# Optimization experiments

Measured on AMD Instinct MI355X. Metric: run time of the kernel, lower is better.

Reference implementation:

```python
import jax, jax.numpy as jnp
import numpy as np

N_NODES = 50000
N_EDGES = 800000
N_GRAPHS = 64
IN_DIM, HID1, HID2, N_CLASSES = 128, 256, 128, 10


def setup_inputs() -> dict:
    key = jax.random.key(0)
    ks = jax.random.split(key, 12)
    x = jax.random.normal(ks[0], (N_NODES, IN_DIM), dtype=jnp.float32)
    src = jax.random.randint(ks[1], (N_EDGES,), 0, N_NODES, dtype=jnp.int32)
    dst = jax.random.randint(ks[2], (N_EDGES,), 0, N_NODES, dtype=jnp.int32)
    graph_id = jnp.sort(jax.random.randint(ks[3], (N_NODES,), 0, N_GRAPHS, dtype=jnp.int32))
    s1 = 1.0 / np.sqrt(IN_DIM)
    s2 = 1.0 / np.sqrt(HID1)
    s3 = 1.0 / np.sqrt(HID2)
    s4 = 1.0 / np.sqrt(12)
    return {
        'x': x, 'src': src, 'dst': dst, 'graph_id': graph_id,
        'W1': jax.random.normal(ks[4], (IN_DIM, HID1), dtype=jnp.float32) * s1,
        'b1': jnp.zeros((HID1,), dtype=jnp.float32),
        'W2': jax.random.normal(ks[5], (HID1, HID2), dtype=jnp.float32) * s2,
        'b2': jnp.zeros((HID2,), dtype=jnp.float32),
        'Wc1': jax.random.normal(ks[6], (HID2, 12), dtype=jnp.float32) * s3,
        'bc1': jnp.zeros((12,), dtype=jnp.float32),
        'Wc2': jax.random.normal(ks[7], (12, 12), dtype=jnp.float32) * s4,
        'bc2': jnp.zeros((12,), dtype=jnp.float32),
        'Wc3': jax.random.normal(ks[8], (12, N_CLASSES), dtype=jnp.float32) * s4,
        'bc3': jnp.zeros((N_CLASSES,), dtype=jnp.float32),
    }


def _graph_conv(x, W, b, src, dst, inv_sqrt_out, inv_sqrt_in, n_nodes):
    # DGL GraphConv, norm='both': D_out^{-1/2} applied to source feats,
    # sum-aggregate over edges, then D_in^{-1/2} on destination, then +bias.
    # Weight applied first (equivalent by linearity; reduces gather traffic
    # when out_dim < in_dim, and is exactly what DGL does in that case).
    xw = (x * inv_sqrt_out[:, None]) @ W                      # [N, out]
    agg = jax.ops.segment_sum(xw[src], dst, num_segments=n_nodes)  # SpMM
    return agg * inv_sqrt_in[:, None] + b


def reference(x, src, dst, graph_id, W1, b1, W2, b2, Wc1, bc1, Wc2, bc2, Wc3, bc3):
    n = x.shape[0]
    ones_e = jnp.ones(src.shape, dtype=x.dtype)
    deg_out = jnp.maximum(jax.ops.segment_sum(ones_e, src, num_segments=n), 1.0)
    deg_in = jnp.maximum(jax.ops.segment_sum(ones_e, dst, num_segments=n), 1.0)
    inv_o = jax.lax.rsqrt(deg_out)
    inv_i = jax.lax.rsqrt(deg_in)

    h = jax.nn.relu(_graph_conv(x, W1, b1, src, dst, inv_o, inv_i, n))
    h = jax.nn.relu(_graph_conv(h, W2, b2, src, dst, inv_o, inv_i, n))

    # dgl.mean_nodes: per-graph mean over nodes of the batched graph
    gsum = jax.ops.segment_sum(h, graph_id, num_segments=N_GRAPHS)   # [G, HID2]
    cnt = jnp.maximum(jax.ops.segment_sum(jnp.ones((n,), dtype=h.dtype), graph_id, num_segments=N_GRAPHS), 1.0)
    hg = gsum / cnt[:, None]

    # tiny 3-layer MLP (no activations in between, as in the source)
    out = hg @ Wc1 + bc1
    out = out @ Wc2 + bc2
    out = out @ Wc3 + bc3
    return out
```

## Files before the change

kernel.cpp:

```cpp
#include <hip/hip_runtime.h>
#include <hip/hip_bf16.h>

#define IN_DIM 128
#define HID1 256
#define HID2 128

#define HB_BINS 25000
#define HB_WORDS 12500
#define HB_CHUNKS 64
__global__ __launch_bounds__(256) void hist_count(const int* __restrict__ src,
                                                  const int* __restrict__ dst,
                                                  int E, int chunk_size,
                                                  int* __restrict__ part_in,
                                                  int* __restrict__ part_out, int N) {
    __shared__ int sm[HB_WORDS];
    const int* idx = (blockIdx.z == 0) ? dst : src;
    int* part = (blockIdx.z == 0) ? part_in : part_out;
    const int base = blockIdx.y * HB_BINS;
    const int ebeg = blockIdx.x * chunk_size;
    const int eend = min(ebeg + chunk_size, E);
    for (int w = threadIdx.x; w < HB_WORDS; w += 256) sm[w] = 0;
    __syncthreads();
    for (int e = ebeg + threadIdx.x; e < eend; e += 256) {
        int v = idx[e] - base;
        if ((unsigned)v < (unsigned)HB_BINS)
            atomicAdd(&sm[v >> 1], 1 << ((v & 1) * 16));
    }
    __syncthreads();
    const int nb = min(HB_BINS, N - base);
    int* dp = part + (size_t)blockIdx.x * N + base;
    for (int w = threadIdx.x; 2 * w < nb; w += 256) {
        int packed = sm[w];
        int b = 2 * w;
        dp[b] = packed & 0xffff;
        if (b + 1 < nb) dp[b + 1] = (packed >> 16) & 0xffff;
    }
}

__global__ __launch_bounds__(256) void hist_reduce(const int* __restrict__ part_in,
                                                   const int* __restrict__ part_out,
                                                   int N, int* __restrict__ deg_in,
                                                   float* __restrict__ inv_i,
                                                   float* __restrict__ inv_o) {
    int b = blockIdx.x * blockDim.x + threadIdx.x;
    if (b >= N) return;
    int di = 0, dox = 0;
#pragma unroll 4
    for (int k = 0; k < HB_CHUNKS; ++k) {
        di += part_in[(size_t)k * N + b];
        dox += part_out[(size_t)k * N + b];
    }
    deg_in[b] = di;
    inv_i[b] = rsqrtf((float)max(di, 1));
    inv_o[b] = rsqrtf((float)max(dox, 1));
}

#define SCAN_B 256
__global__ __launch_bounds__(SCAN_B) void scan_partial(const int* __restrict__ deg,
                                                       int* __restrict__ blockSums, int n) {
    __shared__ int sm[SCAN_B];
    int i = blockIdx.x * SCAN_B + threadIdx.x;
    int v = (i < n) ? deg[i] : 0;
    sm[threadIdx.x] = v;
    __syncthreads();
#pragma unroll
    for (int off = SCAN_B / 2; off > 0; off >>= 1) {
        if (threadIdx.x < off) sm[threadIdx.x] += sm[threadIdx.x + off];
        __syncthreads();
    }
    if (threadIdx.x == 0) blockSums[blockIdx.x] = sm[0];
}

__global__ __launch_bounds__(SCAN_B) void scan_blocksums(int* __restrict__ blockSums, int nb) {
    __shared__ int sm[SCAN_B];
    int t = threadIdx.x;
    int v = (t < nb) ? blockSums[t] : 0;
    sm[t] = v;
    __syncthreads();
#pragma unroll
    for (int off = 1; off < SCAN_B; off <<= 1) {
        int u = (t >= off) ? sm[t - off] : 0;
        __syncthreads();
        sm[t] += u;
        __syncthreads();
    }
    if (t < nb) blockSums[t] = sm[t] - v;
}

__global__ __launch_bounds__(SCAN_B) void scan_final(const int* __restrict__ deg,
                                                     const int* __restrict__ blockSums,
                                                     int* __restrict__ row, int n) {
    __shared__ int sm[SCAN_B];
    int i = blockIdx.x * SCAN_B + threadIdx.x;
    int v = (i < n) ? deg[i] : 0;
    sm[threadIdx.x] = v;
    __syncthreads();
#pragma unroll
    for (int off = 1; off < SCAN_B; off <<= 1) {
        int u = (threadIdx.x >= off) ? sm[threadIdx.x - off] : 0;
        __syncthreads();
        sm[threadIdx.x] += u;
        __syncthreads();
    }
    int excl = sm[threadIdx.x] - v + blockSums[blockIdx.x];
    if (i < n) {
        row[i] = excl;
        if (i == n - 1) row[n] = excl + v;
    }
}

#define BK_SHIFT 8
#define NBUCK 196
#define NCHUNK 256
__global__ __launch_bounds__(256) void coarse_hist(const int* __restrict__ dst, int E,
                                                   int chunk_size, int* __restrict__ ccnt) {
    __shared__ int cnt[NBUCK];
    for (int i = threadIdx.x; i < NBUCK; i += 256) cnt[i] = 0;
    __syncthreads();
    int ebeg = blockIdx.x * chunk_size, eend = min(ebeg + chunk_size, E);
    for (int e = ebeg + threadIdx.x; e < eend; e += 256)
        atomicAdd(&cnt[dst[e] >> BK_SHIFT], 1);
    __syncthreads();
    for (int i = threadIdx.x; i < NBUCK; i += 256) ccnt[blockIdx.x * NBUCK + i] = cnt[i];
}

__global__ __launch_bounds__(NCHUNK) void coarse_off(const int* __restrict__ ccnt,
                                                     const int* __restrict__ row, int N,
                                                     int* __restrict__ coff) {
    __shared__ int sm[NCHUNK];
    int b = blockIdx.x, t = threadIdx.x;
    int v = ccnt[t * NBUCK + b];
    sm[t] = v;
    __syncthreads();
#pragma unroll
    for (int off = 1; off < NCHUNK; off <<= 1) {
        int u = (t >= off) ? sm[t - off] : 0;
        __syncthreads();
        sm[t] += u;
        __syncthreads();
    }
    int base = row[min(b << BK_SHIFT, N)];
    coff[t * NBUCK + b] = base + sm[t] - v;
}

__global__ __launch_bounds__(256) void scat_a(const int* __restrict__ src,
                                              const int* __restrict__ dst, int E,
                                              int chunk_size, const int* __restrict__ coff,
                                              int2* __restrict__ pairs) {
    __shared__ int lcur[NBUCK];
    for (int i = threadIdx.x; i < NBUCK; i += 256) lcur[i] = coff[blockIdx.x * NBUCK + i];
    __syncthreads();
    int ebeg = blockIdx.x * chunk_size, eend = min(ebeg + chunk_size, E);
    for (int e = ebeg + threadIdx.x; e < eend; e += 256) {
        int d = dst[e];
        int p = atomicAdd(&lcur[d >> BK_SHIFT], 1);
        pairs[p] = make_int2(src[e], d);
    }
}

__global__ __launch_bounds__(256) void scat_b(const int2* __restrict__ pairs,
                                              const int* __restrict__ row, int N,
                                              int* __restrict__ csr_src) {
    __shared__ int cur[1 << BK_SHIFT];
    const int nb0 = blockIdx.x << BK_SHIFT;
    const int nb1 = min(nb0 + (1 << BK_SHIFT), N);
    if (nb0 >= N) return;
    for (int i = threadIdx.x; i < nb1 - nb0; i += 256) cur[i] = row[nb0 + i];
    __syncthreads();
    const int beg = row[nb0], end = row[nb1];
    for (int j = beg + threadIdx.x; j < end; j += 256) {
        int2 pr = pairs[j];
        int p = atomicAdd(&cur[pr.y - nb0], 1);
        csr_src[p] = pr.x;
    }
}

__global__ void cvt_kernel(const float* __restrict__ in, __hip_bfloat16* __restrict__ out, int n4) {
    int i = blockIdx.x * blockDim.x + threadIdx.x;
    if (i < n4) {
        float4 v = reinterpret_cast<const float4*>(in)[i];
        __hip_bfloat16 b0 = __float2bfloat16(v.x);
        __hip_bfloat16 b1 = __float2bfloat16(v.y);
        __hip_bfloat16 b2 = __float2bfloat16(v.z);
        __hip_bfloat16 b3 = __float2bfloat16(v.w);
        ushort4 o = make_ushort4(*(unsigned short*)&b0, *(unsigned short*)&b1,
                                 *(unsigned short*)&b2, *(unsigned short*)&b3);
        reinterpret_cast<ushort4*>(out)[i] = o;
    }
}

__global__ void cvt_transpose_kernel(const float* __restrict__ W, __hip_bfloat16* __restrict__ Wt,
                                     int K, int N) {
    int idx = blockIdx.x * blockDim.x + threadIdx.x;
    if (idx < K * N) {
        int k = idx / N;
        int n = idx - k * N;
        Wt[n * K + k] = __float2bfloat16(W[idx]);
    }
}

__device__ __forceinline__ void bf2_unpack(unsigned int p, float& lo, float& hi) {
    lo = __uint_as_float(p << 16);
    hi = __uint_as_float(p & 0xffff0000u);
}

__global__ __launch_bounds__(256) void spmm_kernel(const __hip_bfloat16* __restrict__ feat,
                                                   const float* __restrict__ scale,
                                                   const int* __restrict__ row,
                                                   const int* __restrict__ csr_src,
                                                   __hip_bfloat16* __restrict__ out_bf,
                                                   float* __restrict__ out_f32, int N) {
    const int node = blockIdx.x * 4 + (threadIdx.x >> 6);
    if (node >= N) return;
    const int lane = threadIdx.x & 63;
    const unsigned int* fp = (const unsigned int*)feat;
    const int beg = row[node];
    const int end = row[node + 1];
    float a0 = 0.f, a1 = 0.f;
    int j = beg;
    if (scale) {
        for (; j + 4 <= end; j += 4) {
            int s0 = csr_src[j], s1 = csr_src[j + 1], s2 = csr_src[j + 2], s3 = csr_src[j + 3];
            unsigned int p0 = fp[(size_t)s0 * 64 + lane];
            unsigned int p1 = fp[(size_t)s1 * 64 + lane];
            unsigned int p2 = fp[(size_t)s2 * 64 + lane];
            unsigned int p3 = fp[(size_t)s3 * 64 + lane];
            float c0 = scale[s0], c1 = scale[s1], c2 = scale[s2], c3 = scale[s3];
            float lo, hi;
            bf2_unpack(p0, lo, hi); a0 += lo * c0; a1 += hi * c0;
            bf2_unpack(p1, lo, hi); a0 += lo * c1; a1 += hi * c1;
            bf2_unpack(p2, lo, hi); a0 += lo * c2; a1 += hi * c2;
            bf2_unpack(p3, lo, hi); a0 += lo * c3; a1 += hi * c3;
        }
        for (; j < end; ++j) {
            int s0 = csr_src[j];
            unsigned int p0 = fp[(size_t)s0 * 64 + lane];
            float c0 = scale[s0], lo, hi;
            bf2_unpack(p0, lo, hi); a0 += lo * c0; a1 += hi * c0;
        }
    } else {
        for (; j + 4 <= end; j += 4) {
            int s0 = csr_src[j], s1 = csr_src[j + 1], s2 = csr_src[j + 2], s3 = csr_src[j + 3];
            unsigned int p0 = fp[(size_t)s0 * 64 + lane];
            unsigned int p1 = fp[(size_t)s1 * 64 + lane];
            unsigned int p2 = fp[(size_t)s2 * 64 + lane];
            unsigned int p3 = fp[(size_t)s3 * 64 + lane];
            float lo, hi;
            bf2_unpack(p0, lo, hi); a0 += lo; a1 += hi;
            bf2_unpack(p1, lo, hi); a0 += lo; a1 += hi;
            bf2_unpack(p2, lo, hi); a0 += lo; a1 += hi;
            bf2_unpack(p3, lo, hi); a0 += lo; a1 += hi;
        }
        for (; j < end; ++j) {
            unsigned int p0 = fp[(size_t)csr_src[j] * 64 + lane];
            float lo, hi;
            bf2_unpack(p0, lo, hi); a0 += lo; a1 += hi;
        }
    }
    if (out_bf) {
        __hip_bfloat16 b0 = __float2bfloat16(a0);
        __hip_bfloat16 b1 = __float2bfloat16(a1);
        unsigned int packed = (unsigned int)(*(unsigned short*)&b0) |
                              ((unsigned int)(*(unsigned short*)&b1) << 16);
        ((unsigned int*)out_bf)[(size_t)node * 64 + lane] = packed;
    } else {
        float2 o = make_float2(a0, a1);
        ((float2*)out_f32)[(size_t)node * 64 + lane] = o;
    }
}

#define GBM 128
#define GBN 128
#define GBK 32
#define LPAD 40
typedef __attribute__((ext_vector_type(4))) float floatx4;
typedef __attribute__((ext_vector_type(8))) short shortx8;

__global__ __launch_bounds__(256) void mfma_gemm_kernel(const __hip_bfloat16* __restrict__ A,
                                                        const __hip_bfloat16* __restrict__ Bt,
                                                        __hip_bfloat16* __restrict__ C,
                                                        const float* __restrict__ scaleR,
                                                        const float* __restrict__ bias,
                                                        const float* __restrict__ scaleO,
                                                        int M, int Nn, int K, int doRelu) {
    __shared__ __align__(16) __hip_bfloat16 As[GBM * LPAD];
    __shared__ __align__(16) __hip_bfloat16 Bs[GBN * LPAD];
    const int tid = threadIdx.x;
    const int bm = blockIdx.x * GBM;
    const int bn = blockIdx.y * GBN;
    const int wid = tid >> 6;
    const int lane = tid & 63;
    const int wm = (wid & 1) * 64;
    const int wn = (wid >> 1) * 64;
    const int lrow = lane & 15;
    const int quad = lane >> 4;

    floatx4 acc[4][4] = {};

    for (int k0 = 0; k0 < K; k0 += GBK) {
#pragma unroll
        for (int it = 0; it < 2; ++it) {
            int slot = tid + (it << 8);
            int r = slot >> 2;
            int c = (slot & 3) << 3;
            int gr = bm + r;
            float4 v = make_float4(0.f, 0.f, 0.f, 0.f);
            if (gr < M) v = *reinterpret_cast<const float4*>(A + (size_t)gr * K + k0 + c);
            *reinterpret_cast<float4*>(&As[r * LPAD + c]) = v;
        }
#pragma unroll
        for (int it = 0; it < 2; ++it) {
            int slot = tid + (it << 8);
            int r = slot >> 2;
            int c = (slot & 3) << 3;
            float4 v = *reinterpret_cast<const float4*>(Bt + (size_t)(bn + r) * K + k0 + c);
            *reinterpret_cast<float4*>(&Bs[r * LPAD + c]) = v;
        }
        __syncthreads();

        shortx8 af[4], bf[4];
#pragma unroll
        for (int i = 0; i < 4; ++i)
            af[i] = *reinterpret_cast<const shortx8*>(&As[(wm + i * 16 + lrow) * LPAD + quad * 8]);
#pragma unroll
        for (int i = 0; i < 4; ++i)
            bf[i] = *reinterpret_cast<const shortx8*>(&Bs[(wn + i * 16 + lrow) * LPAD + quad * 8]);
#pragma unroll
        for (int im = 0; im < 4; ++im)
#pragma unroll
            for (int in = 0; in < 4; ++in)
                acc[im][in] = __builtin_amdgcn_mfma_f32_16x16x32_bf16(af[im], bf[in], acc[im][in], 0, 0, 0);
        __syncthreads();
    }

    float bv[4];
#pragma unroll
    for (int in = 0; in < 4; ++in)
        bv[in] = bias ? bias[bn + wn + in * 16 + lrow] : 0.f;

#pragma unroll
    for (int im = 0; im < 4; ++im) {
#pragma unroll
        for (int reg = 0; reg < 4; ++reg) {
            int r = bm + wm + im * 16 + quad * 4 + reg;
            if (r >= M) continue;
            float sR = scaleR ? scaleR[r] : 1.f;
            float sO = scaleO ? scaleO[r] : 1.f;
#pragma unroll
            for (int in = 0; in < 4; ++in) {
                int c = bn + wn + in * 16 + lrow;
                float v = acc[im][in][reg] * sR + bv[in];
                if (doRelu) v = fmaxf(v, 0.f);
                v *= sO;
                C[(size_t)r * Nn + c] = __float2bfloat16(v);
            }
        }
    }
}

#define POOL_CHUNK 64
__global__ __launch_bounds__(128) void pool_kernel(const float* __restrict__ agg2,
                                                   const float* __restrict__ inv_i,
                                                   const float* __restrict__ b2,
                                                   const int* __restrict__ graph_id,
                                                   int n, float* __restrict__ hg_sum) {
    const int f = threadIdx.x;
    const int beg = blockIdx.x * POOL_CHUNK;
    const int end = min(beg + POOL_CHUNK, n);
    if (beg >= n) return;
    const float bias = b2[f];
    int g = graph_id[beg];
    float acc = 0.f;
    for (int i = beg; i < end; ++i) {
        int gi = graph_id[i];
        if (gi != g) {
            atomicAdd(&hg_sum[g * HID2 + f], acc);
            acc = 0.f;
            g = gi;
        }
        float v = agg2[(size_t)i * HID2 + f] * inv_i[i] + bias;
        acc += fmaxf(v, 0.f);
    }
    atomicAdd(&hg_sum[g * HID2 + f], acc);
}

__device__ __forceinline__ int lower_bound_i(const int* a, int n, int key) {
    int lo = 0, hi = n;
    while (lo < hi) {
        int mid = (lo + hi) >> 1;
        if (a[mid] < key) lo = mid + 1; else hi = mid;
    }
    return lo;
}

__global__ __launch_bounds__(64) void mlp_kernel(const float* __restrict__ hg_sum,
                                                 const int* __restrict__ graph_id, int n,
                                                 const float* __restrict__ Wc1, const float* __restrict__ bc1,
                                                 const float* __restrict__ Wc2, const float* __restrict__ bc2,
                                                 const float* __restrict__ Wc3, const float* __restrict__ bc3,
                                                 float* __restrict__ out) {
    const int g = blockIdx.x;
    const int t = threadIdx.x;
    __shared__ float h[HID2];
    __shared__ float t1[12];
    __shared__ float t2[12];
    __shared__ float s_inv_cnt;
    if (t == 0) {
        int beg = lower_bound_i(graph_id, n, g);
        int end = lower_bound_i(graph_id, n, g + 1);
        int c = end - beg;
        s_inv_cnt = 1.0f / (float)max(c, 1);
    }
    __syncthreads();
    const float ic = s_inv_cnt;
    for (int i = t; i < HID2; i += 64) h[i] = hg_sum[g * HID2 + i] * ic;
    __syncthreads();
    if (t < 12) {
        float a = bc1[t];
        for (int k = 0; k < HID2; ++k) a += h[k] * Wc1[k * 12 + t];
        t1[t] = a;
    }
    __syncthreads();
    if (t < 12) {
        float a = bc2[t];
        for (int k = 0; k < 12; ++k) a += t1[k] * Wc2[k * 12 + t];
        t2[t] = a;
    }
    __syncthreads();
    if (t < 10) {
        float a = bc3[t];
        for (int k = 0; k < 12; ++k) a += t2[k] * Wc3[k * 10 + t];
        out[g * 10 + t] = a;
    }
}

extern "C" void kernel_launch(void* const* d_in, const int* in_sizes, int n_in,
                              void* d_out, int out_size, void* d_ws, size_t ws_size,
                              hipStream_t stream) {
    const float* x        = (const float*)d_in[0];
    const int*   src      = (const int*)d_in[1];
    const int*   dst      = (const int*)d_in[2];
    const int*   graph_id = (const int*)d_in[3];
    const float* W1       = (const float*)d_in[4];
    const float* b1       = (const float*)d_in[5];
    const float* W2       = (const float*)d_in[6];
    const float* b2       = (const float*)d_in[7];
    const float* Wc1      = (const float*)d_in[8];
    const float* bc1      = (const float*)d_in[9];
    const float* Wc2      = (const float*)d_in[10];
    const float* bc2      = (const float*)d_in[11];
    const float* Wc3      = (const float*)d_in[12];
    const float* bc3      = (const float*)d_in[13];
    float* out = (float*)d_out;

    const int N = in_sizes[0] / IN_DIM;
    const int E = in_sizes[1];
    const int G = out_size / 10;

    char* ws = (char*)d_ws;
    size_t off = 0;
    auto alloc = [&](size_t bytes) -> char* {
        char* p = ws + off;
        off = (off + bytes + 255) & ~(size_t)255;
        return p;
    };
    const int NB = (N + SCAN_B - 1) / SCAN_B;
    int*   deg_in  = (int*)alloc((size_t)N * 4);
    float* inv_i   = (float*)alloc((size_t)N * 4);
    float* inv_o   = (float*)alloc((size_t)N * 4);
    int*   row     = (int*)alloc((size_t)(N + 1) * 4);
    int*   bsums   = (int*)alloc((size_t)NB * 4);
    int*   ccnt    = (int*)alloc((size_t)NCHUNK * NBUCK * 4);
    int*   coff    = (int*)alloc((size_t)NCHUNK * NBUCK * 4);
    int2*  pairs   = (int2*)alloc((size_t)E * 8);
    int*   csr_src = (int*)alloc((size_t)E * 4);
    float* hg      = (float*)alloc((size_t)G * HID2 * 4);
    __hip_bfloat16* x_bf    = (__hip_bfloat16*)alloc((size_t)N * IN_DIM * 2);
    __hip_bfloat16* W1t     = (__hip_bfloat16*)alloc((size_t)IN_DIM * HID1 * 2);
    __hip_bfloat16* W2t     = (__hip_bfloat16*)alloc((size_t)HID1 * HID2 * 2);
    __hip_bfloat16* agg1_bf = (__hip_bfloat16*)alloc((size_t)N * IN_DIM * 2);
    __hip_bfloat16* h1_bf   = (__hip_bfloat16*)alloc((size_t)N * HID1 * 2);
    __hip_bfloat16* xw2_bf  = (__hip_bfloat16*)alloc((size_t)N * HID2 * 2);
    float* agg2    = (float*)alloc((size_t)N * HID2 * 4);

    int* part_in  = (int*)h1_bf;
    int* part_out = part_in + (size_t)HB_CHUNKS * N;

    hipMemsetAsync(hg, 0, (size_t)G * HID2 * 4, stream);

    const int hchunk = (E + HB_CHUNKS - 1) / HB_CHUNKS;
    const int n_ranges = (N + HB_BINS - 1) / HB_BINS;
    hist_count<<<dim3(HB_CHUNKS, n_ranges, 2), 256, 0, stream>>>(src, dst, E, hchunk,
                                                                 part_in, part_out, N);
    hist_reduce<<<(N + 255) / 256, 256, 0, stream>>>(part_in, part_out, N, deg_in, inv_i, inv_o);
    scan_partial<<<NB, SCAN_B, 0, stream>>>(deg_in, bsums, N);
    scan_blocksums<<<1, SCAN_B, 0, stream>>>(bsums, NB);
    scan_final<<<NB, SCAN_B, 0, stream>>>(deg_in, bsums, row, N);

    const int schunk = (E + NCHUNK - 1) / NCHUNK;
    coarse_hist<<<NCHUNK, 256, 0, stream>>>(dst, E, schunk, ccnt);
    coarse_off<<<NBUCK, NCHUNK, 0, stream>>>(ccnt, row, N, coff);
    scat_a<<<NCHUNK, 256, 0, stream>>>(src, dst, E, schunk, coff, pairs);
    scat_b<<<NBUCK, 256, 0, stream>>>(pairs, row, N, csr_src);

    cvt_kernel<<<(N * IN_DIM / 4 + 255) / 256, 256, 0, stream>>>(x, x_bf, N * IN_DIM / 4);
    cvt_transpose_kernel<<<(IN_DIM * HID1 + 255) / 256, 256, 0, stream>>>(W1, W1t, IN_DIM, HID1);
    cvt_transpose_kernel<<<(HID1 * HID2 + 255) / 256, 256, 0, stream>>>(W2, W2t, HID1, HID2);

    spmm_kernel<<<(N + 3) / 4, 256, 0, stream>>>(x_bf, inv_o, row, csr_src, agg1_bf, nullptr, N);
    mfma_gemm_kernel<<<dim3((N + GBM - 1) / GBM, HID1 / GBN), 256, 0, stream>>>(
        agg1_bf, W1t, h1_bf, inv_i, b1, inv_o, N, HID1, IN_DIM, 1);

    mfma_gemm_kernel<<<dim3((N + GBM - 1) / GBM, HID2 / GBN), 256, 0, stream>>>(
        h1_bf, W2t, xw2_bf, nullptr, nullptr, nullptr, N, HID2, HID1, 0);
    spmm_kernel<<<(N + 3) / 4, 256, 0, stream>>>(xw2_bf, nullptr, row, csr_src, nullptr, agg2, N);

    pool_kernel<<<(N + POOL_CHUNK - 1) / POOL_CHUNK, 128, 0, stream>>>(agg2, inv_i, b2, graph_id, N, hg);
    mlp_kernel<<<G, 64, 0, stream>>>(hg, graph_id, N, Wc1, bc1, Wc2, bc2, Wc3, bc3, out);
}
```

Measured before the change: 305.9 us.

## Fold scale into conversion, fuse scan partial and weight transposes, bf16 agg2

The source-degree scaling moves out of the first SpMM gather and into the x-to-bf16 conversion, so the gather loop no longer loads a per-source scale. The block partial sums of the degree scan are merged into hist_reduce, and the two weight transpose kernels become one launch. The second SpMM now writes bf16 into the reused agg1 buffer instead of a separate fp32 buffer, which halves that write and the pool read. In exchange, agg2 is rounded to bf16 before the final scale, bias and ReLU, which adds a small precision loss.

```diff
diff --git a/kernel.cpp b/kernel.cpp
--- a/kernel.cpp
+++ b/kernel.cpp
@@ -41,36 +41,32 @@
                                                    const int* __restrict__ part_out,
                                                    int N, int* __restrict__ deg_in,
                                                    float* __restrict__ inv_i,
-                                                   float* __restrict__ inv_o) {
-    int b = blockIdx.x * blockDim.x + threadIdx.x;
-    if (b >= N) return;
+                                                   float* __restrict__ inv_o,
+                                                   int* __restrict__ blockSums) {
+    __shared__ int sm[256];
+    int b = blockIdx.x * 256 + threadIdx.x;
     int di = 0, dox = 0;
+    if (b < N) {
 #pragma unroll 4
-    for (int k = 0; k < HB_CHUNKS; ++k) {
-        di += part_in[(size_t)k * N + b];
-        dox += part_out[(size_t)k * N + b];
-    }
-    deg_in[b] = di;
-    inv_i[b] = rsqrtf((float)max(di, 1));
-    inv_o[b] = rsqrtf((float)max(dox, 1));
+        for (int k = 0; k < HB_CHUNKS; ++k) {
+            di += part_in[(size_t)k * N + b];
+            dox += part_out[(size_t)k * N + b];
+        }
+        deg_in[b] = di;
+        inv_i[b] = rsqrtf((float)max(di, 1));
+        inv_o[b] = rsqrtf((float)max(dox, 1));
+    }
+    sm[threadIdx.x] = di;
+    __syncthreads();
+#pragma unroll
+    for (int off = 128; off > 0; off >>= 1) {
+        if (threadIdx.x < off) sm[threadIdx.x] += sm[threadIdx.x + off];
+        __syncthreads();
+    }
+    if (threadIdx.x == 0) blockSums[blockIdx.x] = sm[0];
 }
 
 #define SCAN_B 256
-__global__ __launch_bounds__(SCAN_B) void scan_partial(const int* __restrict__ deg,
-                                                       int* __restrict__ blockSums, int n) {
-    __shared__ int sm[SCAN_B];
-    int i = blockIdx.x * SCAN_B + threadIdx.x;
-    int v = (i < n) ? deg[i] : 0;
-    sm[threadIdx.x] = v;
-    __syncthreads();
-#pragma unroll
-    for (int off = SCAN_B / 2; off > 0; off >>= 1) {
-        if (threadIdx.x < off) sm[threadIdx.x] += sm[threadIdx.x + off];
-        __syncthreads();
-    }
-    if (threadIdx.x == 0) blockSums[blockIdx.x] = sm[0];
-}
-
 __global__ __launch_bounds__(SCAN_B) void scan_blocksums(int* __restrict__ blockSums, int nb) {
     __shared__ int sm[SCAN_B];
     int t = threadIdx.x;
@@ -175,27 +171,34 @@
     }
 }
 
-__global__ void cvt_kernel(const float* __restrict__ in, __hip_bfloat16* __restrict__ out, int n4) {
+__global__ void cvt_scale_kernel(const float* __restrict__ in,
+                                 const float* __restrict__ rowscale,
+                                 __hip_bfloat16* __restrict__ out, int n4) {
     int i = blockIdx.x * blockDim.x + threadIdx.x;
     if (i < n4) {
+        float s = rowscale[i >> 5];
         float4 v = reinterpret_cast<const float4*>(in)[i];
-        __hip_bfloat16 b0 = __float2bfloat16(v.x);
-        __hip_bfloat16 b1 = __float2bfloat16(v.y);
-        __hip_bfloat16 b2 = __float2bfloat16(v.z);
-        __hip_bfloat16 b3 = __float2bfloat16(v.w);
+        __hip_bfloat16 b0 = __float2bfloat16(v.x * s);
+        __hip_bfloat16 b1 = __float2bfloat16(v.y * s);
+        __hip_bfloat16 b2 = __float2bfloat16(v.z * s);
+        __hip_bfloat16 b3 = __float2bfloat16(v.w * s);
         ushort4 o = make_ushort4(*(unsigned short*)&b0, *(unsigned short*)&b1,
                                  *(unsigned short*)&b2, *(unsigned short*)&b3);
         reinterpret_cast<ushort4*>(out)[i] = o;
     }
 }
 
-__global__ void cvt_transpose_kernel(const float* __restrict__ W, __hip_bfloat16* __restrict__ Wt,
-                                     int K, int N) {
+__global__ void cvt_transpose2_kernel(const float* __restrict__ W1, __hip_bfloat16* __restrict__ W1t,
+                                      const float* __restrict__ W2, __hip_bfloat16* __restrict__ W2t) {
     int idx = blockIdx.x * blockDim.x + threadIdx.x;
-    if (idx < K * N) {
-        int k = idx / N;
-        int n = idx - k * N;
-        Wt[n * K + k] = __float2bfloat16(W[idx]);
+    const int S1 = IN_DIM * HID1;
+    if (idx < S1) {
+        int k = idx / HID1, n = idx - k * HID1;
+        W1t[n * IN_DIM + k] = __float2bfloat16(W1[idx]);
+    } else if (idx < S1 + HID1 * HID2) {
+        int j = idx - S1;
+        int k = j / HID2, n = j - k * HID2;
+        W2t[n * HID1 + k] = __float2bfloat16(W2[j]);
     }
 }
 
@@ -205,11 +208,9 @@
 }
 
 __global__ __launch_bounds__(256) void spmm_kernel(const __hip_bfloat16* __restrict__ feat,
-                                                   const float* __restrict__ scale,
                                                    const int* __restrict__ row,
                                                    const int* __restrict__ csr_src,
-                                                   __hip_bfloat16* __restrict__ out_bf,
-                                                   float* __restrict__ out_f32, int N) {
+                                                   __hip_bfloat16* __restrict__ out_bf, int N) {
     const int node = blockIdx.x * 4 + (threadIdx.x >> 6);
     if (node >= N) return;
     const int lane = threadIdx.x & 63;
@@ -218,55 +219,28 @@
     const int end = row[node + 1];
     float a0 = 0.f, a1 = 0.f;
     int j = beg;
-    if (scale) {
-        for (; j + 4 <= end; j += 4) {
-            int s0 = csr_src[j], s1 = csr_src[j + 1], s2 = csr_src[j + 2], s3 = csr_src[j + 3];
-            unsigned int p0 = fp[(size_t)s0 * 64 + lane];
-            unsigned int p1 = fp[(size_t)s1 * 64 + lane];
-            unsigned int p2 = fp[(size_t)s2 * 64 + lane];
-            unsigned int p3 = fp[(size_t)s3 * 64 + lane];
-            float c0 = scale[s0], c1 = scale[s1], c2 = scale[s2], c3 = scale[s3];
-            float lo, hi;
-            bf2_unpack(p0, lo, hi); a0 += lo * c0; a1 += hi * c0;
-            bf2_unpack(p1, lo, hi); a0 += lo * c1; a1 += hi * c1;
-            bf2_unpack(p2, lo, hi); a0 += lo * c2; a1 += hi * c2;
-            bf2_unpack(p3, lo, hi); a0 += lo * c3; a1 += hi * c3;
-        }
-        for (; j < end; ++j) {
-            int s0 = csr_src[j];
-            unsigned int p0 = fp[(size_t)s0 * 64 + lane];
-            float c0 = scale[s0], lo, hi;
-            bf2_unpack(p0, lo, hi); a0 += lo * c0; a1 += hi * c0;
-        }
-    } else {
-        for (; j + 4 <= end; j += 4) {
-            int s0 = csr_src[j], s1 = csr_src[j + 1], s2 = csr_src[j + 2], s3 = csr_src[j + 3];
-            unsigned int p0 = fp[(size_t)s0 * 64 + lane];
-            unsigned int p1 = fp[(size_t)s1 * 64 + lane];
-            unsigned int p2 = fp[(size_t)s2 * 64 + lane];
-            unsigned int p3 = fp[(size_t)s3 * 64 + lane];
-            float lo, hi;
-            bf2_unpack(p0, lo, hi); a0 += lo; a1 += hi;
-            bf2_unpack(p1, lo, hi); a0 += lo; a1 += hi;
-            bf2_unpack(p2, lo, hi); a0 += lo; a1 += hi;
-            bf2_unpack(p3, lo, hi); a0 += lo; a1 += hi;
-        }
-        for (; j < end; ++j) {
-            unsigned int p0 = fp[(size_t)csr_src[j] * 64 + lane];
-            float lo, hi;
-            bf2_unpack(p0, lo, hi); a0 += lo; a1 += hi;
-        }
-    }
-    if (out_bf) {
-        __hip_bfloat16 b0 = __float2bfloat16(a0);
-        __hip_bfloat16 b1 = __float2bfloat16(a1);
-        unsigned int packed = (unsigned int)(*(unsigned short*)&b0) |
-                              ((unsigned int)(*(unsigned short*)&b1) << 16);
-        ((unsigned int*)out_bf)[(size_t)node * 64 + lane] = packed;
-    } else {
-        float2 o = make_float2(a0, a1);
-        ((float2*)out_f32)[(size_t)node * 64 + lane] = o;
-    }
+    for (; j + 4 <= end; j += 4) {
+        int s0 = csr_src[j], s1 = csr_src[j + 1], s2 = csr_src[j + 2], s3 = csr_src[j + 3];
+        unsigned int p0 = fp[(size_t)s0 * 64 + lane];
+        unsigned int p1 = fp[(size_t)s1 * 64 + lane];
+        unsigned int p2 = fp[(size_t)s2 * 64 + lane];
+        unsigned int p3 = fp[(size_t)s3 * 64 + lane];
+        float lo, hi;
+        bf2_unpack(p0, lo, hi); a0 += lo; a1 += hi;
+        bf2_unpack(p1, lo, hi); a0 += lo; a1 += hi;
+        bf2_unpack(p2, lo, hi); a0 += lo; a1 += hi;
+        bf2_unpack(p3, lo, hi); a0 += lo; a1 += hi;
+    }
+    for (; j < end; ++j) {
+        unsigned int p0 = fp[(size_t)csr_src[j] * 64 + lane];
+        float lo, hi;
+        bf2_unpack(p0, lo, hi); a0 += lo; a1 += hi;
+    }
+    __hip_bfloat16 b0 = __float2bfloat16(a0);
+    __hip_bfloat16 b1 = __float2bfloat16(a1);
+    unsigned int packed = (unsigned int)(*(unsigned short*)&b0) |
+                          ((unsigned int)(*(unsigned short*)&b1) << 16);
+    ((unsigned int*)out_bf)[(size_t)node * 64 + lane] = packed;
 }
 
 #define GBM 128
@@ -359,7 +333,7 @@
 }
 
 #define POOL_CHUNK 64
-__global__ __launch_bounds__(128) void pool_kernel(const float* __restrict__ agg2,
+__global__ __launch_bounds__(128) void pool_kernel(const __hip_bfloat16* __restrict__ agg2,
                                                    const float* __restrict__ inv_i,
                                                    const float* __restrict__ b2,
                                                    const int* __restrict__ graph_id,
@@ -368,6 +342,7 @@
     const int beg = blockIdx.x * POOL_CHUNK;
     const int end = min(beg + POOL_CHUNK, n);
     if (beg >= n) return;
+    const unsigned short* ap = (const unsigned short*)agg2;
     const float bias = b2[f];
     int g = graph_id[beg];
     float acc = 0.f;
@@ -378,7 +353,8 @@
             acc = 0.f;
             g = gi;
         }
-        float v = agg2[(size_t)i * HID2 + f] * inv_i[i] + bias;
+        float a = __uint_as_float((unsigned int)ap[(size_t)i * HID2 + f] << 16);
+        float v = a * inv_i[i] + bias;
         acc += fmaxf(v, 0.f);
     }
     atomicAdd(&hg_sum[g * HID2 + f], acc);
@@ -481,7 +457,7 @@
     __hip_bfloat16* agg1_bf = (__hip_bfloat16*)alloc((size_t)N * IN_DIM * 2);
     __hip_bfloat16* h1_bf   = (__hip_bfloat16*)alloc((size_t)N * HID1 * 2);
     __hip_bfloat16* xw2_bf  = (__hip_bfloat16*)alloc((size_t)N * HID2 * 2);
-    float* agg2    = (float*)alloc((size_t)N * HID2 * 4);
+    __hip_bfloat16* agg2_bf = agg1_bf;
 
     int* part_in  = (int*)h1_bf;
     int* part_out = part_in + (size_t)HB_CHUNKS * N;
@@ -492,8 +468,7 @@
     const int n_ranges = (N + HB_BINS - 1) / HB_BINS;
     hist_count<<<dim3(HB_CHUNKS, n_ranges, 2), 256, 0, stream>>>(src, dst, E, hchunk,
                                                                  part_in, part_out, N);
-    hist_reduce<<<(N + 255) / 256, 256, 0, stream>>>(part_in, part_out, N, deg_in, inv_i, inv_o);
-    scan_partial<<<NB, SCAN_B, 0, stream>>>(deg_in, bsums, N);
+    hist_reduce<<<NB, 256, 0, stream>>>(part_in, part_out, N, deg_in, inv_i, inv_o, bsums);
     scan_blocksums<<<1, SCAN_B, 0, stream>>>(bsums, NB);
     scan_final<<<NB, SCAN_B, 0, stream>>>(deg_in, bsums, row, N);
 
@@ -503,18 +478,17 @@
     scat_a<<<NCHUNK, 256, 0, stream>>>(src, dst, E, schunk, coff, pairs);
     scat_b<<<NBUCK, 256, 0, stream>>>(pairs, row, N, csr_src);
 
-    cvt_kernel<<<(N * IN_DIM / 4 + 255) / 256, 256, 0, stream>>>(x, x_bf, N * IN_DIM / 4);
-    cvt_transpose_kernel<<<(IN_DIM * HID1 + 255) / 256, 256, 0, stream>>>(W1, W1t, IN_DIM, HID1);
-    cvt_transpose_kernel<<<(HID1 * HID2 + 255) / 256, 256, 0, stream>>>(W2, W2t, HID1, HID2);
-
-    spmm_kernel<<<(N + 3) / 4, 256, 0, stream>>>(x_bf, inv_o, row, csr_src, agg1_bf, nullptr, N);
+    cvt_scale_kernel<<<(N * IN_DIM / 4 + 255) / 256, 256, 0, stream>>>(x, inv_o, x_bf, N * IN_DIM / 4);
+    cvt_transpose2_kernel<<<(IN_DIM * HID1 + HID1 * HID2 + 255) / 256, 256, 0, stream>>>(W1, W1t, W2, W2t);
+
+    spmm_kernel<<<(N + 3) / 4, 256, 0, stream>>>(x_bf, row, csr_src, agg1_bf, N);
     mfma_gemm_kernel<<<dim3((N + GBM - 1) / GBM, HID1 / GBN), 256, 0, stream>>>(
         agg1_bf, W1t, h1_bf, inv_i, b1, inv_o, N, HID1, IN_DIM, 1);
 
     mfma_gemm_kernel<<<dim3((N + GBM - 1) / GBM, HID2 / GBN), 256, 0, stream>>>(
         h1_bf, W2t, xw2_bf, nullptr, nullptr, nullptr, N, HID2, HID1, 0);
-    spmm_kernel<<<(N + 3) / 4, 256, 0, stream>>>(xw2_bf, nullptr, row, csr_src, nullptr, agg2, N);
-
-    pool_kernel<<<(N + POOL_CHUNK - 1) / POOL_CHUNK, 128, 0, stream>>>(agg2, inv_i, b2, graph_id, N, hg);
+    spmm_kernel<<<(N + 3) / 4, 256, 0, stream>>>(xw2_bf, row, csr_src, agg2_bf, N);
+
+    pool_kernel<<<(N + POOL_CHUNK - 1) / POOL_CHUNK, 128, 0, stream>>>(agg2_bf, inv_i, b2, graph_id, N, hg);
     mlp_kernel<<<G, 64, 0, stream>>>(hg, graph_id, N, Wc1, bc1, Wc2, bc2, Wc3, bc3, out);
 }
```

Result: no change. 302.8 us (-1.0%).
